# Kernel optimization log

Measured on AMD Instinct MI355X. Metric: run time of the kernel, lower is better.

Reference implementation:

```python
import jax, jax.numpy as jnp
import numpy as np

# --- constants matching vis_net(scale=1) ---
SCALE = 1.0
L = 8                      # n_levels
F = 2                      # n_features_per_level
LOG2_T = 19
T = 1 << LOG2_T            # hash table size per level
N_MIN = 32                 # base_resolution
B = float(np.exp(np.log(2048.0 * SCALE / N_MIN) / (L - 1)))  # per_level_scale

PRIMES = jnp.array([1, 2654435761, 805459861], dtype=jnp.uint32)
# 8 corners of the unit cube
OFFSETS = jnp.array([[(c >> d) & 1 for d in range(3)] for c in range(8)], dtype=jnp.uint32)  # [8,3]


def _hash(coords):
    # coords: [N,8,3] uint32 -> [N,8] int32 indices into table of size T
    h = coords * PRIMES                      # uint32 wraps, as in tcnn
    h = h[..., 0] ^ h[..., 1] ^ h[..., 2]
    return (h & jnp.uint32(T - 1)).astype(jnp.int32)


def _encode(x01, table):
    # x01: [N,3] in [0,1]; table: [L,T,F]
    feats = []
    for l in range(L):
        scale_l = N_MIN * (B ** l) - 1.0     # tcnn grid scale for level l
        pos = x01 * scale_l + 0.5            # [N,3]
        p0 = jnp.floor(pos)
        w = pos - p0                         # trilinear fractions [N,3]
        corners = p0.astype(jnp.uint32)[:, None, :] + OFFSETS[None, :, :]  # [N,8,3]
        idx = _hash(corners)                 # [N,8]
        f = table[l][idx]                    # gather -> [N,8,F]
        wt = jnp.prod(jnp.where(OFFSETS[None].astype(bool), w[:, None, :], 1.0 - w[:, None, :]), axis=-1)  # [N,8]
        feats.append(jnp.sum(f * wt[..., None], axis=1))  # [N,F]
    return jnp.concatenate(feats, axis=-1)   # [N, L*F] = [N,16]


def setup_inputs() -> dict:
    key = jax.random.key(0)
    k0, k1, k2, k3 = jax.random.split(key, 4)
    N = 4_194_304
    x = jax.random.uniform(k0, (N, 3), jnp.float32, -SCALE, SCALE)
    # tcnn initializes hash features uniform in [-1e-4, 1e-4]
    table = jax.random.uniform(k1, (L, T, F), jnp.float32, -1e-4, 1e-4)
    W1 = jax.random.normal(k2, (L * F, 32), jnp.float32) * (1.0 / np.sqrt(L * F))
    b1 = jnp.zeros((32,), jnp.float32)
    W2 = jax.random.normal(k3, (32, 1), jnp.float32) * (1.0 / np.sqrt(32))
    b2 = jnp.zeros((1,), jnp.float32)
    return {"x": x, "table": table, "W1": W1, "b1": b1, "W2": W2, "b2": b2}


def reference(x, table, W1, b1, W2, b2):
    # normalize to [0,1] as in forward: (x - xyz_min) / (xyz_max - xyz_min)
    x01 = (x + SCALE) / (2.0 * SCALE)
    enc = _encode(x01, table)                      # [N,16]
    h = jax.nn.relu(enc @ W1 + b1)                 # [N,32]
    vis = jax.nn.sigmoid(h @ W2 + b2)              # [N,1]
    return vis[:, 0]
```

## Files before the change

### kernel.cpp

```cpp
#include <hip/hip_runtime.h>
#include <hip/hip_bf16.h>
#include <math.h>

#define NLVL 8
#define LOG2T 19
#define TSZ (1u << LOG2T)

typedef float f32x2 __attribute__((ext_vector_type(2)));

struct Scales { float s[NLVL]; };

static __device__ __forceinline__ unsigned short f2bf(float f) {
    unsigned u = __builtin_bit_cast(unsigned, f);
    u += 0x7fffu + ((u >> 16) & 1u);
    return (unsigned short)(u >> 16);
}
static __device__ __forceinline__ float bfbits2f(unsigned hi16) {
    return __builtin_bit_cast(float, hi16);
}

__global__ __launch_bounds__(256) void encode_kernel(
    const float* __restrict__ x,
    const float* __restrict__ table,
    unsigned* __restrict__ encb,
    int N, Scales sc)
{
    const int lvl = blockIdx.x & 7;
    const int i = (blockIdx.x >> 3) * blockDim.x + threadIdx.x;
    if (i >= N) return;

    float xx = __builtin_nontemporal_load(x + 3 * i + 0);
    float yy = __builtin_nontemporal_load(x + 3 * i + 1);
    float zz = __builtin_nontemporal_load(x + 3 * i + 2);
    float px = (xx + 1.0f) * 0.5f;
    float py = (yy + 1.0f) * 0.5f;
    float pz = (zz + 1.0f) * 0.5f;

    const float s = sc.s[lvl];
    float fx = fmaf(px, s, 0.5f);
    float fy = fmaf(py, s, 0.5f);
    float fz = fmaf(pz, s, 0.5f);
    float bx = floorf(fx), by = floorf(fy), bz = floorf(fz);
    float wx = fx - bx, wy = fy - by, wz = fz - bz;
    unsigned cx = (unsigned)bx, cy = (unsigned)by, cz = (unsigned)bz;

    unsigned hy0 = cy * 2654435761u;
    unsigned hy1 = hy0 + 2654435761u;
    unsigned hz0 = cz * 805459861u;
    unsigned hz1 = hz0 + 805459861u;
    unsigned cx1 = cx + 1u;
    const unsigned m = TSZ - 1u;
    const f32x2* tl = reinterpret_cast<const f32x2*>(table) + (size_t)lvl * TSZ;

    f32x2 f000 = tl[(cx  ^ hy0 ^ hz0) & m];
    f32x2 f100 = tl[(cx1 ^ hy0 ^ hz0) & m];
    f32x2 f010 = tl[(cx  ^ hy1 ^ hz0) & m];
    f32x2 f110 = tl[(cx1 ^ hy1 ^ hz0) & m];
    f32x2 f001 = tl[(cx  ^ hy0 ^ hz1) & m];
    f32x2 f101 = tl[(cx1 ^ hy0 ^ hz1) & m];
    f32x2 f011 = tl[(cx  ^ hy1 ^ hz1) & m];
    f32x2 f111 = tl[(cx1 ^ hy1 ^ hz1) & m];

    float wx0 = 1.0f - wx, wy0 = 1.0f - wy, wz0 = 1.0f - wz;
    float w00 = wx0 * wy0, w10 = wx * wy0, w01 = wx0 * wy, w11 = wx * wy;
    float a000 = w00 * wz0, a100 = w10 * wz0, a010 = w01 * wz0, a110 = w11 * wz0;
    float a001 = w00 * wz,  a101 = w10 * wz,  a011 = w01 * wz,  a111 = w11 * wz;

    float e0 = fmaf(f000.x, a000,
               fmaf(f100.x, a100,
               fmaf(f010.x, a010,
               fmaf(f110.x, a110,
               fmaf(f001.x, a001,
               fmaf(f101.x, a101,
               fmaf(f011.x, a011, f111.x * a111)))))));
    float e1 = fmaf(f000.y, a000,
               fmaf(f100.y, a100,
               fmaf(f010.y, a010,
               fmaf(f110.y, a110,
               fmaf(f001.y, a001,
               fmaf(f101.y, a101,
               fmaf(f011.y, a011, f111.y * a111)))))));

    unsigned pk = ((unsigned)f2bf(e1) << 16) | (unsigned)f2bf(e0);
    __builtin_nontemporal_store(pk, encb + (size_t)lvl * N + i);
}

__global__ __launch_bounds__(256) void mlp_kernel(
    const unsigned* __restrict__ encb,
    const float* __restrict__ W1,
    const float* __restrict__ b1,
    const float* __restrict__ W2,
    const float* __restrict__ b2,
    float* __restrict__ out, int N)
{
    int i = blockIdx.x * blockDim.x + threadIdx.x;
    if (i >= N) return;

    float enc[16];
    #pragma unroll
    for (int l = 0; l < NLVL; ++l) {
        unsigned pk = __builtin_nontemporal_load(encb + (size_t)l * N + i);
        enc[2 * l + 0] = bfbits2f(pk << 16);
        enc[2 * l + 1] = bfbits2f(pk & 0xffff0000u);
    }

    float h[32];
    #pragma unroll
    for (int j = 0; j < 32; ++j) h[j] = b1[j];
    #pragma unroll
    for (int k = 0; k < 16; ++k) {
        float e = enc[k];
        #pragma unroll
        for (int j = 0; j < 32; ++j)
            h[j] = fmaf(e, W1[k * 32 + j], h[j]);
    }
    float z = b2[0];
    #pragma unroll
    for (int j = 0; j < 32; ++j)
        z = fmaf(fmaxf(h[j], 0.0f), W2[j], z);

    out[i] = 1.0f / (1.0f + __expf(-z));
}

__global__ __launch_bounds__(256) void fused_kernel(
    const float* __restrict__ x, const float* __restrict__ table,
    const float* __restrict__ W1, const float* __restrict__ b1,
    const float* __restrict__ W2, const float* __restrict__ b2,
    float* __restrict__ out, int N, Scales sc)
{
    int i = blockIdx.x * blockDim.x + threadIdx.x;
    if (i >= N) return;
    float px = (x[3 * i + 0] + 1.0f) * 0.5f;
    float py = (x[3 * i + 1] + 1.0f) * 0.5f;
    float pz = (x[3 * i + 2] + 1.0f) * 0.5f;
    float enc[16];
    #pragma unroll
    for (int l = 0; l < NLVL; ++l) {
        const float s = sc.s[l];
        float fx = fmaf(px, s, 0.5f), fy = fmaf(py, s, 0.5f), fz = fmaf(pz, s, 0.5f);
        float bx = floorf(fx), by = floorf(fy), bz = floorf(fz);
        float wx = fx - bx, wy = fy - by, wz = fz - bz;
        unsigned cx = (unsigned)bx, cy = (unsigned)by, cz = (unsigned)bz;
        unsigned hy0 = cy * 2654435761u, hy1 = hy0 + 2654435761u;
        unsigned hz0 = cz * 805459861u, hz1 = hz0 + 805459861u;
        unsigned cx1 = cx + 1u;
        const unsigned m = TSZ - 1u;
        const f32x2* tl = reinterpret_cast<const f32x2*>(table) + (size_t)l * TSZ;
        f32x2 f000 = tl[(cx ^ hy0 ^ hz0) & m], f100 = tl[(cx1 ^ hy0 ^ hz0) & m];
        f32x2 f010 = tl[(cx ^ hy1 ^ hz0) & m], f110 = tl[(cx1 ^ hy1 ^ hz0) & m];
        f32x2 f001 = tl[(cx ^ hy0 ^ hz1) & m], f101 = tl[(cx1 ^ hy0 ^ hz1) & m];
        f32x2 f011 = tl[(cx ^ hy1 ^ hz1) & m], f111 = tl[(cx1 ^ hy1 ^ hz1) & m];
        float wx0 = 1.0f - wx, wy0 = 1.0f - wy, wz0 = 1.0f - wz;
        float w00 = wx0 * wy0, w10 = wx * wy0, w01 = wx0 * wy, w11 = wx * wy;
        float a000 = w00 * wz0, a100 = w10 * wz0, a010 = w01 * wz0, a110 = w11 * wz0;
        float a001 = w00 * wz, a101 = w10 * wz, a011 = w01 * wz, a111 = w11 * wz;
        enc[2*l+0] = fmaf(f000.x,a000, fmaf(f100.x,a100, fmaf(f010.x,a010, fmaf(f110.x,a110,
                     fmaf(f001.x,a001, fmaf(f101.x,a101, fmaf(f011.x,a011, f111.x*a111)))))));
        enc[2*l+1] = fmaf(f000.y,a000, fmaf(f100.y,a100, fmaf(f010.y,a010, fmaf(f110.y,a110,
                     fmaf(f001.y,a001, fmaf(f101.y,a101, fmaf(f011.y,a011, f111.y*a111)))))));
    }
    float h[32];
    #pragma unroll
    for (int j = 0; j < 32; ++j) h[j] = b1[j];
    #pragma unroll
    for (int k = 0; k < 16; ++k) {
        float e = enc[k];
        #pragma unroll
        for (int j = 0; j < 32; ++j) h[j] = fmaf(e, W1[k * 32 + j], h[j]);
    }
    float z = b2[0];
    #pragma unroll
    for (int j = 0; j < 32; ++j) z = fmaf(fmaxf(h[j], 0.0f), W2[j], z);
    out[i] = 1.0f / (1.0f + __expf(-z));
}

extern "C" void kernel_launch(void* const* d_in, const int* in_sizes, int n_in,
                              void* d_out, int out_size, void* d_ws, size_t ws_size,
                              hipStream_t stream) {
    const float* x     = (const float*)d_in[0];
    const float* table = (const float*)d_in[1];
    const float* W1    = (const float*)d_in[2];
    const float* b1    = (const float*)d_in[3];
    const float* W2    = (const float*)d_in[4];
    const float* b2    = (const float*)d_in[5];
    float* out = (float*)d_out;

    int N = in_sizes[0] / 3;

    Scales sc;
    double B = exp(log(2048.0 / 32.0) / 7.0);
    for (int l = 0; l < NLVL; ++l)
        sc.s[l] = (float)(32.0 * pow(B, (double)l) - 1.0);

    const int block = 256;
    const int chunks = (N + block - 1) / block;
    size_t need = (size_t)NLVL * (size_t)N * sizeof(unsigned);

    if (ws_size >= need) {
        unsigned* encb = (unsigned*)d_ws;
        encode_kernel<<<chunks * NLVL, block, 0, stream>>>(x, table, encb, N, sc);
        mlp_kernel<<<chunks, block, 0, stream>>>(encb, W1, b1, W2, b2, out, N);
    } else {
        fused_kernel<<<chunks, block, 0, stream>>>(x, table, W1, b1, W2, b2, out, N, sc);
    }
}
```

Baseline: 830.5 us.

## Morton-bucket sort points before hash-grid encoding to improve gather locality

Adds a counting sort of input points into 2^18 Morton-ordered buckets (histogram, single-block scan, atomic scatter). The sorted keys drive the encode and MLP kernels, and results are scattered back to the original indices. The aim is to make neighbouring threads hit nearby hash-table entries, cutting random-gather cache misses on the table. In exchange it adds several extra passes, global atomics, a serial-ish single-block scan and scattered output writes. Coordinates are also quantized to 14 bits per axis, which slightly perturbs the interpolation weights.

```diff
diff --git a/kernel.cpp b/kernel.cpp
--- a/kernel.cpp
+++ b/kernel.cpp
@@ -5,8 +5,10 @@
 #define NLVL 8
 #define LOG2T 19
 #define TSZ (1u << LOG2T)
+#define NB (1 << 18)
 
 typedef float f32x2 __attribute__((ext_vector_type(2)));
+typedef unsigned long long u64;
 
 struct Scales { float s[NLVL]; };
 
@@ -18,23 +20,88 @@
 static __device__ __forceinline__ float bfbits2f(unsigned hi16) {
     return __builtin_bit_cast(float, hi16);
 }
-
-__global__ __launch_bounds__(256) void encode_kernel(
-    const float* __restrict__ x,
+static __device__ __forceinline__ unsigned mort6(unsigned a) {
+    return (a & 1) | ((a & 2) << 2) | ((a & 4) << 4) |
+           ((a & 8) << 6) | ((a & 16) << 8) | ((a & 32) << 10);
+}
+static __device__ __forceinline__ void quant_key(float xx, float yy, float zz,
+                                                 unsigned& qx, unsigned& qy, unsigned& qz,
+                                                 unsigned& key) {
+    qx = (unsigned)fminf(fmaf(xx, 8192.0f, 8192.0f), 16383.0f);
+    qy = (unsigned)fminf(fmaf(yy, 8192.0f, 8192.0f), 16383.0f);
+    qz = (unsigned)fminf(fmaf(zz, 8192.0f, 8192.0f), 16383.0f);
+    key = mort6(qx >> 8) | (mort6(qy >> 8) << 1) | (mort6(qz >> 8) << 2);
+}
+
+__global__ __launch_bounds__(256) void hist_kernel(
+    const float* __restrict__ x, unsigned* __restrict__ hist, int N)
+{
+    const int stride = gridDim.x * blockDim.x;
+    for (int i = blockIdx.x * blockDim.x + threadIdx.x; i < N; i += stride) {
+        float xx = __builtin_nontemporal_load(x + 3 * i + 0);
+        float yy = __builtin_nontemporal_load(x + 3 * i + 1);
+        float zz = __builtin_nontemporal_load(x + 3 * i + 2);
+        unsigned qx, qy, qz, key;
+        quant_key(xx, yy, zz, qx, qy, qz, key);
+        atomicAdd(&hist[key], 1u);
+    }
+}
+
+__global__ __launch_bounds__(1024) void scan_kernel(unsigned* __restrict__ hist)
+{
+    __shared__ unsigned sh[1024];
+    const int t = threadIdx.x;
+    const int per = NB / 1024;
+    const int base = t * per;
+    unsigned sum = 0;
+    for (int k = 0; k < per; ++k) sum += hist[base + k];
+    sh[t] = sum;
+    __syncthreads();
+    for (int off = 1; off < 1024; off <<= 1) {
+        unsigned v = (t >= off) ? sh[t - off] : 0u;
+        __syncthreads();
+        sh[t] += v;
+        __syncthreads();
+    }
+    unsigned run = sh[t] - sum;
+    for (int k = 0; k < per; ++k) {
+        unsigned c = hist[base + k];
+        hist[base + k] = run;
+        run += c;
+    }
+}
+
+__global__ __launch_bounds__(256) void scatter_kernel(
+    const float* __restrict__ x, unsigned* __restrict__ hist,
+    u64* __restrict__ skey, int N)
+{
+    const int stride = gridDim.x * blockDim.x;
+    for (int i = blockIdx.x * blockDim.x + threadIdx.x; i < N; i += stride) {
+        float xx = __builtin_nontemporal_load(x + 3 * i + 0);
+        float yy = __builtin_nontemporal_load(x + 3 * i + 1);
+        float zz = __builtin_nontemporal_load(x + 3 * i + 2);
+        unsigned qx, qy, qz, key;
+        quant_key(xx, yy, zz, qx, qy, qz, key);
+        unsigned pos = atomicAdd(&hist[key], 1u);
+        u64 pk = (u64)qx | ((u64)qy << 14) | ((u64)qz << 28) | ((u64)(unsigned)i << 42);
+        skey[pos] = pk;
+    }
+}
+
+__global__ __launch_bounds__(256) void encode_sorted_kernel(
+    const u64* __restrict__ skey,
     const float* __restrict__ table,
     unsigned* __restrict__ encb,
     int N, Scales sc)
 {
     const int lvl = blockIdx.x & 7;
-    const int i = (blockIdx.x >> 3) * blockDim.x + threadIdx.x;
-    if (i >= N) return;
-
-    float xx = __builtin_nontemporal_load(x + 3 * i + 0);
-    float yy = __builtin_nontemporal_load(x + 3 * i + 1);
-    float zz = __builtin_nontemporal_load(x + 3 * i + 2);
-    float px = (xx + 1.0f) * 0.5f;
-    float py = (yy + 1.0f) * 0.5f;
-    float pz = (zz + 1.0f) * 0.5f;
+    const int j = (blockIdx.x >> 3) * blockDim.x + threadIdx.x;
+    if (j >= N) return;
+
+    u64 sk = __builtin_nontemporal_load(skey + j);
+    float px = (float)(unsigned)(sk & 16383u) * (1.0f / 16384.0f);
+    float py = (float)(unsigned)((sk >> 14) & 16383u) * (1.0f / 16384.0f);
+    float pz = (float)(unsigned)((sk >> 28) & 16383u) * (1.0f / 16384.0f);
 
     const float s = sc.s[lvl];
     float fx = fmaf(px, s, 0.5f);
@@ -66,20 +133,96 @@
     float a000 = w00 * wz0, a100 = w10 * wz0, a010 = w01 * wz0, a110 = w11 * wz0;
     float a001 = w00 * wz,  a101 = w10 * wz,  a011 = w01 * wz,  a111 = w11 * wz;
 
-    float e0 = fmaf(f000.x, a000,
-               fmaf(f100.x, a100,
-               fmaf(f010.x, a010,
-               fmaf(f110.x, a110,
-               fmaf(f001.x, a001,
-               fmaf(f101.x, a101,
+    float e0 = fmaf(f000.x, a000, fmaf(f100.x, a100, fmaf(f010.x, a010,
+               fmaf(f110.x, a110, fmaf(f001.x, a001, fmaf(f101.x, a101,
                fmaf(f011.x, a011, f111.x * a111)))))));
-    float e1 = fmaf(f000.y, a000,
-               fmaf(f100.y, a100,
-               fmaf(f010.y, a010,
-               fmaf(f110.y, a110,
-               fmaf(f001.y, a001,
-               fmaf(f101.y, a101,
+    float e1 = fmaf(f000.y, a000, fmaf(f100.y, a100, fmaf(f010.y, a010,
+               fmaf(f110.y, a110, fmaf(f001.y, a001, fmaf(f101.y, a101,
                fmaf(f011.y, a011, f111.y * a111)))))));
+
+    unsigned pk = ((unsigned)f2bf(e1) << 16) | (unsigned)f2bf(e0);
+    __builtin_nontemporal_store(pk, encb + (size_t)lvl * N + j);
+}
+
+__global__ __launch_bounds__(256) void mlp_sorted_kernel(
+    const u64* __restrict__ skey,
+    const unsigned* __restrict__ encb,
+    const float* __restrict__ W1, const float* __restrict__ b1,
+    const float* __restrict__ W2, const float* __restrict__ b2,
+    float* __restrict__ out, int N)
+{
+    int j = blockIdx.x * blockDim.x + threadIdx.x;
+    if (j >= N) return;
+
+    u64 sk = __builtin_nontemporal_load(skey + j);
+    unsigned idx = (unsigned)(sk >> 42);
+
+    float enc[16];
+    #pragma unroll
+    for (int l = 0; l < NLVL; ++l) {
+        unsigned pk = __builtin_nontemporal_load(encb + (size_t)l * N + j);
+        enc[2 * l + 0] = bfbits2f(pk << 16);
+        enc[2 * l + 1] = bfbits2f(pk & 0xffff0000u);
+    }
+
+    float h[32];
+    #pragma unroll
+    for (int jj = 0; jj < 32; ++jj) h[jj] = b1[jj];
+    #pragma unroll
+    for (int k = 0; k < 16; ++k) {
+        float e = enc[k];
+        #pragma unroll
+        for (int jj = 0; jj < 32; ++jj)
+            h[jj] = fmaf(e, W1[k * 32 + jj], h[jj]);
+    }
+    float z = b2[0];
+    #pragma unroll
+    for (int jj = 0; jj < 32; ++jj)
+        z = fmaf(fmaxf(h[jj], 0.0f), W2[jj], z);
+
+    out[idx] = 1.0f / (1.0f + __expf(-z));
+}
+
+__global__ __launch_bounds__(256) void encode_kernel(
+    const float* __restrict__ x, const float* __restrict__ table,
+    unsigned* __restrict__ encb, int N, Scales sc)
+{
+    const int lvl = blockIdx.x & 7;
+    const int i = (blockIdx.x >> 3) * blockDim.x + threadIdx.x;
+    if (i >= N) return;
+
+    float xx = __builtin_nontemporal_load(x + 3 * i + 0);
+    float yy = __builtin_nontemporal_load(x + 3 * i + 1);
+    float zz = __builtin_nontemporal_load(x + 3 * i + 2);
+    float px = (xx + 1.0f) * 0.5f;
+    float py = (yy + 1.0f) * 0.5f;
+    float pz = (zz + 1.0f) * 0.5f;
+
+    const float s = sc.s[lvl];
+    float fx = fmaf(px, s, 0.5f), fy = fmaf(py, s, 0.5f), fz = fmaf(pz, s, 0.5f);
+    float bx = floorf(fx), by = floorf(fy), bz = floorf(fz);
+    float wx = fx - bx, wy = fy - by, wz = fz - bz;
+    unsigned cx = (unsigned)bx, cy = (unsigned)by, cz = (unsigned)bz;
+    unsigned hy0 = cy * 2654435761u, hy1 = hy0 + 2654435761u;
+    unsigned hz0 = cz * 805459861u, hz1 = hz0 + 805459861u;
+    unsigned cx1 = cx + 1u;
+    const unsigned m = TSZ - 1u;
+    const f32x2* tl = reinterpret_cast<const f32x2*>(table) + (size_t)lvl * TSZ;
+
+    f32x2 f000 = tl[(cx ^ hy0 ^ hz0) & m], f100 = tl[(cx1 ^ hy0 ^ hz0) & m];
+    f32x2 f010 = tl[(cx ^ hy1 ^ hz0) & m], f110 = tl[(cx1 ^ hy1 ^ hz0) & m];
+    f32x2 f001 = tl[(cx ^ hy0 ^ hz1) & m], f101 = tl[(cx1 ^ hy0 ^ hz1) & m];
+    f32x2 f011 = tl[(cx ^ hy1 ^ hz1) & m], f111 = tl[(cx1 ^ hy1 ^ hz1) & m];
+
+    float wx0 = 1.0f - wx, wy0 = 1.0f - wy, wz0 = 1.0f - wz;
+    float w00 = wx0 * wy0, w10 = wx * wy0, w01 = wx0 * wy, w11 = wx * wy;
+    float a000 = w00 * wz0, a100 = w10 * wz0, a010 = w01 * wz0, a110 = w11 * wz0;
+    float a001 = w00 * wz, a101 = w10 * wz, a011 = w01 * wz, a111 = w11 * wz;
+
+    float e0 = fmaf(f000.x,a000, fmaf(f100.x,a100, fmaf(f010.x,a010, fmaf(f110.x,a110,
+               fmaf(f001.x,a001, fmaf(f101.x,a101, fmaf(f011.x,a011, f111.x*a111)))))));
+    float e1 = fmaf(f000.y,a000, fmaf(f100.y,a100, fmaf(f010.y,a010, fmaf(f110.y,a110,
+               fmaf(f001.y,a001, fmaf(f101.y,a101, fmaf(f011.y,a011, f111.y*a111)))))));
 
     unsigned pk = ((unsigned)f2bf(e1) << 16) | (unsigned)f2bf(e0);
     __builtin_nontemporal_store(pk, encb + (size_t)lvl * N + i);
@@ -87,15 +230,12 @@
 
 __global__ __launch_bounds__(256) void mlp_kernel(
     const unsigned* __restrict__ encb,
-    const float* __restrict__ W1,
-    const float* __restrict__ b1,
-    const float* __restrict__ W2,
-    const float* __restrict__ b2,
+    const float* __restrict__ W1, const float* __restrict__ b1,
+    const float* __restrict__ W2, const float* __restrict__ b2,
     float* __restrict__ out, int N)
 {
     int i = blockIdx.x * blockDim.x + threadIdx.x;
     if (i >= N) return;
-
     float enc[16];
     #pragma unroll
     for (int l = 0; l < NLVL; ++l) {
@@ -103,7 +243,6 @@
         enc[2 * l + 0] = bfbits2f(pk << 16);
         enc[2 * l + 1] = bfbits2f(pk & 0xffff0000u);
     }
-
     float h[32];
     #pragma unroll
     for (int j = 0; j < 32; ++j) h[j] = b1[j];
@@ -111,14 +250,11 @@
     for (int k = 0; k < 16; ++k) {
         float e = enc[k];
         #pragma unroll
-        for (int j = 0; j < 32; ++j)
-            h[j] = fmaf(e, W1[k * 32 + j], h[j]);
+        for (int j = 0; j < 32; ++j) h[j] = fmaf(e, W1[k * 32 + j], h[j]);
     }
     float z = b2[0];
     #pragma unroll
-    for (int j = 0; j < 32; ++j)
-        z = fmaf(fmaxf(h[j], 0.0f), W2[j], z);
-
+    for (int j = 0; j < 32; ++j) z = fmaf(fmaxf(h[j], 0.0f), W2[j], z);
     out[i] = 1.0f / (1.0f + __expf(-z));
 }
 
@@ -194,9 +330,23 @@
 
     const int block = 256;
     const int chunks = (N + block - 1) / block;
-    size_t need = (size_t)NLVL * (size_t)N * sizeof(unsigned);
-
-    if (ws_size >= need) {
+    const size_t encb_bytes = (size_t)NLVL * N * 4;
+    const size_t skey_bytes = (size_t)N * 8;
+    const size_t hist_bytes = (size_t)NB * 4;
+    const size_t need_sorted = encb_bytes + skey_bytes + hist_bytes;
+
+    if (ws_size >= need_sorted && N <= (1 << 22)) {
+        unsigned* encb = (unsigned*)d_ws;
+        u64* skey = (u64*)((char*)d_ws + encb_bytes);
+        unsigned* hist = (unsigned*)((char*)d_ws + encb_bytes + skey_bytes);
+
+        hipMemsetAsync(hist, 0, hist_bytes, stream);
+        hist_kernel<<<2048, block, 0, stream>>>(x, hist, N);
+        scan_kernel<<<1, 1024, 0, stream>>>(hist);
+        scatter_kernel<<<2048, block, 0, stream>>>(x, hist, skey, N);
+        encode_sorted_kernel<<<chunks * NLVL, block, 0, stream>>>(skey, table, encb, N, sc);
+        mlp_sorted_kernel<<<chunks, block, 0, stream>>>(skey, encb, W1, b1, W2, b2, out, N);
+    } else if (ws_size >= encb_bytes) {
         unsigned* encb = (unsigned*)d_ws;
         encode_kernel<<<chunks * NLVL, block, 0, stream>>>(x, table, encb, N, sc);
         mlp_kernel<<<chunks, block, 0, stream>>>(encb, W1, b1, W2, b2, out, N);
```

Result: slower. 1.408 ms (+69.6%).
